# Optimization experiments

Measured on AMD Instinct MI355X. Metric: run time of the kernel, lower is better.

The kernel has to match this reference:

```python
import jax, jax.numpy as jnp
import numpy as np

RADIUS = 0.2
K = 32       # nsample
S = 1024     # npoint
BN_EPS = 1e-5


def fps(xyz, s):
    # xyz: [B, N, 3] -> indices [B, s] (farthest point sampling, start at index 0)
    B, N, _ = xyz.shape

    def step(carry, _):
        dist, last = carry                                  # [B,N], [B]
        lp = jnp.take_along_axis(xyz, last[:, None, None], axis=1)  # [B,1,3]
        d = jnp.sum((xyz - lp) ** 2, axis=-1)               # [B,N]
        dist = jnp.minimum(dist, d)
        nxt = jnp.argmax(dist, axis=-1).astype(jnp.int32)
        return (dist, nxt), last

    init = (jnp.full((B, N), jnp.inf, xyz.dtype), jnp.zeros((B,), jnp.int32))
    _, idxs = jax.lax.scan(step, init, None, length=s)      # [s, B]
    return idxs.T                                           # [B, s]


def query_ball(new_xyz, xyz, radius, k):
    # new_xyz: [B,S,3], xyz: [B,N,3] -> first k in-ball indices [B,S,k]
    B, N, _ = xyz.shape
    d2 = jnp.sum((new_xyz[:, :, None, :] - xyz[:, None, :, :]) ** 2, axis=-1)  # [B,S,N]
    cand = jnp.where(d2 <= radius * radius, jnp.arange(N, dtype=jnp.int32)[None, None, :], N)
    idx = jnp.sort(cand, axis=-1)[..., :k]                  # first-k by index, pytorch3d order
    first = idx[..., :1]
    idx = jnp.where(idx == N, first, idx)                   # replicate first valid index
    return jnp.minimum(idx, N - 1)


def gather_pts(pts, idx):
    # pts: [B,N,C], idx: [B,S,K] -> [B,S,K,C]
    B, N, C = pts.shape
    _, s, k = idx.shape
    g = jnp.take_along_axis(pts, idx.reshape(B, s * k, 1), axis=1)
    return g.reshape(B, s, k, C)


def conv_bn_relu(x, W, b, g, be):
    # x: [B,S,K,Cin], W: [Cout,Cin] (1x1 conv), training-mode BatchNorm over (B,S,K)
    y = jnp.einsum('bskc,oc->bsko', x, W) + b
    mu = jnp.mean(y, axis=(0, 1, 2))
    var = jnp.var(y, axis=(0, 1, 2))
    y = (y - mu) * jax.lax.rsqrt(var + BN_EPS) * g + be
    return jax.nn.relu(y)


def setup_inputs() -> dict:
    key = jax.random.key(0)
    ks = jax.random.split(key, 8)
    B, N, D = 8, 8192, 64
    inp = {
        'xyz': jax.random.uniform(ks[0], (B, 3, N), dtype=jnp.float32),
        'points': jax.random.normal(ks[1], (B, D, N), dtype=jnp.float32),
    }
    dims = [(64, 67), (64, 64), (128, 64)]
    for i, (o, c) in enumerate(dims):
        inp[f'W{i}'] = jax.random.normal(ks[2 + i], (o, c), dtype=jnp.float32) * 0.05
        inp[f'b{i}'] = jnp.zeros((o,), jnp.float32)
        inp[f'g{i}'] = jnp.ones((o,), jnp.float32)
        inp[f'be{i}'] = jnp.zeros((o,), jnp.float32)
    return inp


def reference(xyz, points, W0, b0, g0, be0, W1, b1, g1, be1, W2, b2, g2, be2):
    # xyz: [B,3,N], points: [B,D,N]
    xyz_n = jnp.transpose(xyz, (0, 2, 1))                   # [B,N,3]
    pts_n = jnp.transpose(points, (0, 2, 1))                # [B,N,D]
    idx = fps(xyz_n, S)                                     # [B,S]
    new_xyz = jnp.take_along_axis(xyz_n, idx[..., None], axis=1)  # [B,S,3]
    gidx = query_ball(new_xyz, xyz_n, RADIUS, K)            # [B,S,K]
    gxyz = (gather_pts(xyz_n, gidx) - new_xyz[:, :, None, :]) / RADIUS  # [B,S,K,3]
    gpts = gather_pts(pts_n, gidx)                          # [B,S,K,D]
    feat = jnp.concatenate([gpts, gxyz], axis=-1)           # [B,S,K,D+3]
    feat = conv_bn_relu(feat, W0, b0, g0, be0)
    feat = conv_bn_relu(feat, W1, b1, g1, be1)
    feat = conv_bn_relu(feat, W2, b2, g2, be2)
    new_points = jnp.max(feat, axis=2)                      # [B,S,Cout]
    return (jnp.transpose(new_xyz, (0, 2, 1)), jnp.transpose(new_points, (0, 2, 1)))
```

## Files before the change

kernel.cpp:

```cpp
#include <hip/hip_runtime.h>

#define BB 8
#define NN 8192
#define SS 1024
#define KK 32
#define NPIX (BB*SS*KK)
#define R2C 0.04f
#define EPS 1e-5f

#define FT 1024
#define FW (FT/64)
#define PPT (NN/FT)
#define NCELL 4096
#define TBLK 64

typedef float v2f __attribute__((ext_vector_type(2)));

#define OFF_IDX      0u
#define OFF_NEWXYZ   (OFF_IDX + BB*SS*4)
#define OFF_GIDX     (OFF_NEWXYZ + BB*SS*3*4)
#define OFF_XYZN     (OFF_GIDX + BB*SS*KK*4)
#define OFF_PTSN     (OFF_XYZN + BB*NN*3*4)
#define OFF_Y0       (OFF_PTSN + BB*NN*64*4)
#define OFF_Y1       (OFF_Y0 + NPIX*64*2)
#define OFF_MAXMIN   (OFF_Y1 + NPIX*64*2)
#define OFF_P0       (OFF_MAXMIN + BB*SS*128*2*4)
#define OFF_P1       (OFF_P0 + 1024*128*4)
#define OFF_P2       (OFF_P1 + 1024*128*4)
#define OFF_SC       (OFF_P2 + 1024*256*4)

__device__ __forceinline__ unsigned short f2bf(float x){
    unsigned u = __float_as_uint(x);
    unsigned r = (u + 0x7FFFu + ((u >> 16) & 1u)) >> 16;
    return (unsigned short)r;
}
__device__ __forceinline__ float bf2f(unsigned h){
    return __uint_as_float(h << 16);
}
__device__ __forceinline__ float sqdist3(float dx, float dy, float dz){
    return __fadd_rn(__fadd_rn(__fmul_rn(dx,dx), __fmul_rn(dy,dy)), __fmul_rn(dz,dz));
}
__device__ __forceinline__ int spread4(int v){
    return (v&1) | ((v&2)<<2) | ((v&4)<<4) | ((v&8)<<6);
}

template<int CTRL>
__device__ __forceinline__ unsigned long long dpp_max_u64(unsigned long long k){
    int lo = (int)(unsigned)k;
    int hi = (int)(unsigned)(k >> 32);
    int olo = __builtin_amdgcn_update_dpp(0, lo, CTRL, 0xf, 0xf, true);
    int ohi = __builtin_amdgcn_update_dpp(0, hi, CTRL, 0xf, 0xf, true);
    unsigned long long o = ((unsigned long long)(unsigned)ohi << 32) | (unsigned)olo;
    return (o > k) ? o : k;
}
template<int CTRL>
__device__ __forceinline__ float dppf_max(float v){
    int o = __builtin_amdgcn_update_dpp(__float_as_int(v), __float_as_int(v), CTRL, 0xf, 0xf, false);
    return fmaxf(v, __int_as_float(o));
}
template<int CTRL>
__device__ __forceinline__ float dppf_min(float v){
    int o = __builtin_amdgcn_update_dpp(__float_as_int(v), __float_as_int(v), CTRL, 0xf, 0xf, false);
    return fminf(v, __int_as_float(o));
}
template<int CTRL>
__device__ __forceinline__ unsigned dppu_min(unsigned v){
    unsigned o = (unsigned)__builtin_amdgcn_update_dpp((int)v, (int)v, CTRL, 0xf, 0xf, false);
    return min(v, o);
}
template<int CTRL>
__device__ __forceinline__ float dpp_sum_step(float v){
    int o = __builtin_amdgcn_update_dpp(0, __float_as_int(v), CTRL, 0xf, 0xf, true);
    return v + __int_as_float(o);
}
__device__ __forceinline__ float wave_sum_f32(float v){
    v = dpp_sum_step<0x111>(v); v = dpp_sum_step<0x112>(v);
    v = dpp_sum_step<0x114>(v); v = dpp_sum_step<0x118>(v);
    v = dpp_sum_step<0x142>(v); v = dpp_sum_step<0x143>(v);
    return v;
}
__device__ __forceinline__ float grp32_max(float v){
    v = dppf_max<0x111>(v); v = dppf_max<0x112>(v);
    v = dppf_max<0x114>(v); v = dppf_max<0x118>(v);
    v = dppf_max<0x142>(v);
    return v;
}
__device__ __forceinline__ float grp32_min(float v){
    v = dppf_min<0x111>(v); v = dppf_min<0x112>(v);
    v = dppf_min<0x114>(v); v = dppf_min<0x118>(v);
    v = dppf_min<0x142>(v);
    return v;
}
__device__ __forceinline__ float wave_max_f32(float v){
    v = dppf_max<0x111>(v); v = dppf_max<0x112>(v);
    v = dppf_max<0x114>(v); v = dppf_max<0x118>(v);
    v = dppf_max<0x142>(v); v = dppf_max<0x143>(v);
    return v;
}
__device__ __forceinline__ unsigned wave_min_u32(unsigned v){
    v = dppu_min<0x111>(v); v = dppu_min<0x112>(v);
    v = dppu_min<0x114>(v); v = dppu_min<0x118>(v);
    v = dppu_min<0x142>(v); v = dppu_min<0x143>(v);
    return v;
}

__global__ __launch_bounds__(FT) void fps_kernel(const float* __restrict__ xyz,
                                                 const float* __restrict__ pts,
                                                 float* __restrict__ newxyz,
                                                 float* __restrict__ out,
                                                 float* __restrict__ xyz_n,
                                                 float* __restrict__ pts_n){
    __shared__ float sxyz[NN * 3];
    __shared__ int   si[NN];
    __shared__ int   hist[NCELL];
    __shared__ int   waveTot[FW];
    __shared__ unsigned long long slots[2][FW];
    int tid = threadIdx.x;

    if (blockIdx.x >= 8){
        int gid = (blockIdx.x - 8) * FT + tid;
        int b = gid >> 13, i = gid & (NN - 1);
        const float* xb = xyz + (size_t)b * 3 * NN;
        float x = xb[i], y = xb[NN + i], z = xb[2 * NN + i];
        float* xd = xyz_n + ((size_t)b * NN + i) * 3;
        xd[0] = x; xd[1] = y; xd[2] = z;
        const float* pb = pts + (size_t)b * 64 * NN + i;
        float4* pd = (float4*)(pts_n + ((size_t)b * NN + i) * 64);
#pragma unroll
        for (int q = 0; q < 16; ++q){
            float4 v;
            v.x = pb[(q*4+0)*NN]; v.y = pb[(q*4+1)*NN];
            v.z = pb[(q*4+2)*NN]; v.w = pb[(q*4+3)*NN];
            pd[q] = v;
        }
        return;
    }

    int b = blockIdx.x;
    int wave = tid >> 6, lane = tid & 63;
    const float* xb = xyz + (size_t)b * 3 * NN;

    int cell[PPT];
#pragma unroll
    for (int j = 0; j < PPT; ++j){
        int i = tid + j * FT;
        float x = xb[i], y = xb[NN + i], z = xb[2*NN + i];
        sxyz[i*3]   = x; sxyz[i*3+1] = y; sxyz[i*3+2] = z;
        int cx = min(15, max(0, (int)(x * 16.f)));
        int cy = min(15, max(0, (int)(y * 16.f)));
        int cz = min(15, max(0, (int)(z * 16.f)));
        cell[j] = spread4(cx) | (spread4(cy) << 1) | (spread4(cz) << 2);
    }
#pragma unroll
    for (int k = 0; k < NCELL/FT; ++k) hist[tid * (NCELL/FT) + k] = 0;
    __syncthreads();
#pragma unroll
    for (int j = 0; j < PPT; ++j) atomicAdd(&hist[cell[j]], 1);
    __syncthreads();
    {
        int base0 = tid * (NCELL/FT);
        int sum4 = 0;
#pragma unroll
        for (int k = 0; k < NCELL/FT; ++k) sum4 += hist[base0 + k];
        int s = sum4;
#pragma unroll
        for (int m = 1; m < 64; m <<= 1){
            int v = __shfl_up(s, m);
            if (lane >= m) s += v;
        }
        if (lane == 63) waveTot[wave] = s;
        __syncthreads();
        int wbase = 0;
#pragma unroll
        for (int w2 = 0; w2 < FW; ++w2) if (w2 < wave) wbase += waveTot[w2];
        int run = wbase + s - sum4;
#pragma unroll
        for (int k = 0; k < NCELL/FT; ++k){
            int h = hist[base0 + k];
            hist[base0 + k] = run;
            run += h;
        }
    }
    __syncthreads();
#pragma unroll
    for (int j = 0; j < PPT; ++j){
        int pos = atomicAdd(&hist[cell[j]], 1);
        si[pos] = tid + j * FT;
    }
    __syncthreads();
    v2f px[PPT/2], py[PPT/2], pz[PPT/2];
    float dist[PPT];
    int oi[PPT];
    float bxmin =  1e30f, bxmax = -1e30f;
    float bymin =  1e30f, bymax = -1e30f;
    float bzmin =  1e30f, bzmax = -1e30f;
#pragma unroll
    for (int j = 0; j < PPT; ++j){
        int g = si[tid * PPT + j];
        oi[j] = g;
        float x = sxyz[g*3], y = sxyz[g*3+1], z = sxyz[g*3+2];
        px[j>>1][j&1] = x; py[j>>1][j&1] = y; pz[j>>1][j&1] = z;
        bxmin = fminf(bxmin, x); bxmax = fmaxf(bxmax, x);
        bymin = fminf(bymin, y); bymax = fmaxf(bymax, y);
        bzmin = fminf(bzmin, z); bzmax = fmaxf(bzmax, z);
        dist[j] = __int_as_float(0x7f800000);
    }
    __syncthreads();

    float tmax = __int_as_float(0x7f800000);
    int   bidx = 0;
    unsigned long long wkey = 0ull;
    int w = 0;
    for (int t = 0; t < SS; ++t){
        if (tid == 0) hist[t] = w;
        int w3 = w * 3;
        float lx = sxyz[w3], ly = sxyz[w3+1], lz = sxyz[w3+2];
        float cdx = __fsub_rn(lx, fminf(fmaxf(lx, bxmin), bxmax));
        float cdy = __fsub_rn(ly, fminf(fmaxf(ly, bymin), bymax));
        float cdz = __fsub_rn(lz, fminf(fmaxf(lz, bzmin), bzmax));
        float d_bb = sqdist3(cdx, cdy, cdz);
        bool active = d_bb < tmax;
        unsigned long long bal = __ballot(active);
        if (bal){
            if (active){
                {
#pragma clang fp contract(off)
                    v2f lx2 = {lx, lx}, ly2 = {ly, ly}, lz2 = {lz, lz};
#pragma unroll
                    for (int p = 0; p < PPT/2; ++p){
                        v2f dx = px[p] - lx2;
                        v2f dy = py[p] - ly2;
                        v2f dz = pz[p] - lz2;
                        v2f d  = ((dx*dx) + (dy*dy)) + (dz*dz);
                        dist[2*p]   = fminf(dist[2*p],   d[0]);
                        dist[2*p+1] = fminf(dist[2*p+1], d[1]);
                    }
                }
                float m0 = fmaxf(dist[0], dist[1]);
                float m1 = fmaxf(dist[2], dist[3]);
                float m2 = fmaxf(dist[4], dist[5]);
                float m3 = fmaxf(dist[6], dist[7]);
                m0 = fmaxf(m0, m1); m2 = fmaxf(m2, m3);
                float maxd = fmaxf(m0, m2);
                int bo = 0x7fffffff;
#pragma unroll
                for (int j = 0; j < PPT; ++j)
                    if (dist[j] == maxd) bo = min(bo, oi[j]);
                tmax = maxd; bidx = bo;
            }
            float m = wave_max_f32(tmax);
            float sm = __int_as_float(__builtin_amdgcn_readlane(__float_as_int(m), 63));
            unsigned cand = (tmax == sm) ? (unsigned)bidx : 0xFFFFFFFFu;
            cand = wave_min_u32(cand);
            unsigned sidx = (unsigned)__builtin_amdgcn_readlane((int)cand, 63);
            wkey = ((unsigned long long)__float_as_uint(sm) << 32) | (unsigned)(~sidx);
        }
        int cur = t & 1;
        if (lane == 63) slots[cur][wave] = wkey;
        __syncthreads();
        unsigned long long v = (lane < FW) ? slots[cur][lane] : 0ull;
        v = dpp_max_u64<0x111>(v);
        v = dpp_max_u64<0x112>(v);
        v = dpp_max_u64<0x114>(v);
        v = dpp_max_u64<0x118>(v);
        unsigned lo = (unsigned)__builtin_amdgcn_readlane((int)(unsigned)v, 15);
        w = (int)(~lo);
    }
    __syncthreads();
    for (int t2 = tid; t2 < SS; t2 += FT){
        int hw = hist[t2] * 3;
        float x = sxyz[hw], y = sxyz[hw+1], z = sxyz[hw+2];
        out[(size_t)b * 3 * SS + t2]          = x;
        out[(size_t)b * 3 * SS + SS + t2]     = y;
        out[(size_t)b * 3 * SS + 2*SS + t2]   = z;
        float* nw = newxyz + ((size_t)b * SS + t2) * 3;
        nw[0] = x; nw[1] = y; nw[2] = z;
    }
}

__global__ __launch_bounds__(256) void qb_kernel(const float* __restrict__ xyz,
                                                 const float* __restrict__ newxyz,
                                                 int* __restrict__ gidx){
    int wid = (blockIdx.x * 256 + threadIdx.x) >> 6;
    int lane = threadIdx.x & 63;
    int b = wid >> 10;
    const float* nw = newxyz + (size_t)wid * 3;
    float cx = nw[0], cy = nw[1], cz = nw[2];
    const float* xb = xyz + (size_t)b * 3 * NN;
    int total = 0, firstIdx = -1;
    int* gout = gidx + (size_t)wid * KK;
    for (int base = 0; base < NN; base += 64){
        int i = base + lane;
        float dx = __fsub_rn(cx, xb[i]);
        float dy = __fsub_rn(cy, xb[NN + i]);
        float dz = __fsub_rn(cz, xb[2*NN + i]);
        float d2 = sqdist3(dx, dy, dz);
        bool in = (d2 <= R2C);
        unsigned long long m = __ballot(in);
        int pos = total + __popcll(m & ((1ull << lane) - 1ull));
        if (in && pos < KK) gout[pos] = i;
        if (firstIdx < 0 && m) firstIdx = base + (__ffsll((unsigned long long)m) - 1);
        total += __popcll(m);
        if (total >= KK) break;
    }
    if (total < KK){
        int f = (total > 0) ? firstIdx : (NN - 1);
        for (int p = total + lane; p < KK; p += 64) gout[p] = f;
    }
}

__global__ __launch_bounds__(256) void l0_kernel(const float* __restrict__ pts_n,
                                                 const float* __restrict__ xyz_n,
                                                 const float* __restrict__ newxyz,
                                                 const int* __restrict__ gidx,
                                                 const float* __restrict__ W0,
                                                 const float* __restrict__ b0,
                                                 uint4* __restrict__ y0,
                                                 float* __restrict__ part0){
    __shared__ float lsum[4][64][2];
    int tid = threadIdx.x;
    int pixel = blockIdx.x * 256 + tid;
    int sample = pixel >> 5;
    int b = sample >> 10;
    int gi = gidx[pixel];
    int wave = tid >> 6, lane = tid & 63;

    float ff[67];
    const float4* prow = (const float4*)(pts_n + ((size_t)b * NN + gi) * 64);
#pragma unroll
    for (int q = 0; q < 16; ++q){
        float4 v = prow[q];
        ff[q*4] = v.x; ff[q*4+1] = v.y; ff[q*4+2] = v.z; ff[q*4+3] = v.w;
    }
    const float* pr = xyz_n + ((size_t)b * NN + gi) * 3;
    const float* nw = newxyz + (size_t)sample * 3;
    ff[64] = __fsub_rn(pr[0], nw[0]) / 0.2f;
    ff[65] = __fsub_rn(pr[1], nw[1]) / 0.2f;
    ff[66] = __fsub_rn(pr[2], nw[2]) / 0.2f;

    for (int oc = 0; oc < 8; ++oc){
        float acc[8];
#pragma unroll
        for (int j = 0; j < 8; ++j) acc[j] = b0[oc*8+j];
#pragma unroll
        for (int c = 0; c < 67; ++c){
            float fe = ff[c];
#pragma unroll
            for (int j = 0; j < 8; ++j) acc[j] += fe * W0[(oc*8+j)*67 + c];
        }
        uint4 pk;
        unsigned us[8];
#pragma unroll
        for (int j = 0; j < 8; ++j){
            float v = acc[j];
            float s1 = wave_sum_f32(v);
            float s2 = wave_sum_f32(v * v);
            if (lane == 63){ lsum[wave][oc*8+j][0] = s1; lsum[wave][oc*8+j][1] = s2; }
            us[j] = f2bf(v);
        }
        pk.x = us[0] | (us[1] << 16);
        pk.y = us[2] | (us[3] << 16);
        pk.z = us[4] | (us[5] << 16);
        pk.w = us[6] | (us[7] << 16);
        y0[(size_t)pixel * 8 + oc] = pk;
    }
    __syncthreads();
    if (tid < 128){
        float s = lsum[0][tid>>1][tid&1] + lsum[1][tid>>1][tid&1]
                + lsum[2][tid>>1][tid&1] + lsum[3][tid>>1][tid&1];
        part0[(size_t)blockIdx.x * 128 + tid] = s;
    }
}

__global__ __launch_bounds__(256) void l1_kernel(const uint4* __restrict__ y0,
                                                 const float* __restrict__ scale0,
                                                 const float* __restrict__ shift0,
                                                 const float* __restrict__ W1,
                                                 const float* __restrict__ b1,
                                                 uint4* __restrict__ y1,
                                                 float* __restrict__ part1){
    __shared__ float lsum[4][64][2];
    int tid = threadIdx.x;
    int pixel = blockIdx.x * 256 + tid;
    int wave = tid >> 6, lane = tid & 63;

    float x[64];
#pragma unroll
    for (int q = 0; q < 8; ++q){
        uint4 v = y0[(size_t)pixel * 8 + q];
        unsigned w[4] = {v.x, v.y, v.z, v.w};
#pragma unroll
        for (int r = 0; r < 4; ++r){
            int c = q*8 + r*2;
            x[c]   = fmaxf(bf2f(w[r] & 0xFFFFu) * scale0[c]   + shift0[c],   0.f);
            x[c+1] = fmaxf(bf2f(w[r] >> 16)     * scale0[c+1] + shift0[c+1], 0.f);
        }
    }
    for (int oc = 0; oc < 8; ++oc){
        float acc[8];
#pragma unroll
        for (int j = 0; j < 8; ++j) acc[j] = b1[oc*8+j];
#pragma unroll
        for (int c = 0; c < 64; ++c){
            float fe = x[c];
#pragma unroll
            for (int j = 0; j < 8; ++j) acc[j] += fe * W1[(oc*8+j)*64 + c];
        }
        uint4 pk;
        unsigned us[8];
#pragma unroll
        for (int j = 0; j < 8; ++j){
            float v = acc[j];
            float s1 = wave_sum_f32(v);
            float s2 = wave_sum_f32(v * v);
            if (lane == 63){ lsum[wave][oc*8+j][0] = s1; lsum[wave][oc*8+j][1] = s2; }
            us[j] = f2bf(v);
        }
        pk.x = us[0] | (us[1] << 16);
        pk.y = us[2] | (us[3] << 16);
        pk.z = us[4] | (us[5] << 16);
        pk.w = us[6] | (us[7] << 16);
        y1[(size_t)pixel * 8 + oc] = pk;
    }
    __syncthreads();
    if (tid < 128){
        float s = lsum[0][tid>>1][tid&1] + lsum[1][tid>>1][tid&1]
                + lsum[2][tid>>1][tid&1] + lsum[3][tid>>1][tid&1];
        part1[(size_t)blockIdx.x * 128 + tid] = s;
    }
}

__global__ __launch_bounds__(256) void l2_kernel(const uint4* __restrict__ y1,
                                                 const float* __restrict__ scale1,
                                                 const float* __restrict__ shift1,
                                                 const float* __restrict__ W2,
                                                 const float* __restrict__ b2,
                                                 float* __restrict__ maxmin,
                                                 float* __restrict__ part2){
    __shared__ float lsum[4][128][2];
    int tid = threadIdx.x;
    int pixel = blockIdx.x * 256 + tid;
    int sample = pixel >> 5;
    int wave = tid >> 6, lane = tid & 63;

    float x[64];
#pragma unroll
    for (int q = 0; q < 8; ++q){
        uint4 v = y1[(size_t)pixel * 8 + q];
        unsigned w[4] = {v.x, v.y, v.z, v.w};
#pragma unroll
        for (int r = 0; r < 4; ++r){
            int c = q*8 + r*2;
            x[c]   = fmaxf(bf2f(w[r] & 0xFFFFu) * scale1[c]   + shift1[c],   0.f);
            x[c+1] = fmaxf(bf2f(w[r] >> 16)     * scale1[c+1] + shift1[c+1], 0.f);
        }
    }
    for (int oc = 0; oc < 16; ++oc){
        float acc[8];
#pragma unroll
        for (int j = 0; j < 8; ++j) acc[j] = b2[oc*8+j];
#pragma unroll
        for (int c = 0; c < 64; ++c){
            float fe = x[c];
#pragma unroll
            for (int j = 0; j < 8; ++j) acc[j] += fe * W2[(oc*8+j)*64 + c];
        }
#pragma unroll
        for (int j = 0; j < 8; ++j){
            float v = acc[j];
            int ch = oc*8 + j;
            float mx = grp32_max(v);
            float mn = grp32_min(v);
            float s1 = wave_sum_f32(v);
            float s2 = wave_sum_f32(v * v);
            if (lane == 63){ lsum[wave][ch][0] = s1; lsum[wave][ch][1] = s2; }
            if ((tid & 31) == 31){
                float* mm = maxmin + ((size_t)sample * 128 + ch) * 2;
                mm[0] = mx; mm[1] = mn;
            }
        }
    }
    __syncthreads();
    {
        float s = lsum[0][tid>>1][tid&1] + lsum[1][tid>>1][tid&1]
                + lsum[2][tid>>1][tid&1] + lsum[3][tid>>1][tid&1];
        part2[(size_t)blockIdx.x * 256 + tid] = s;
    }
}

__global__ __launch_bounds__(1024) void fin_kernel(const float* __restrict__ part, int O,
                           const float* __restrict__ g, const float* __restrict__ be,
                           float* __restrict__ scale, float* __restrict__ shift){
    __shared__ float4 ls[1024];
    int tid = threadIdx.x;
    int M = 2 * O;
    int V = M >> 2;
    int NC = 1024 / V;
    int q = tid & (V - 1);
    int c = tid / V;
    int per = 1024 / NC;
    const float4* p4 = (const float4*)part;
    float4 s = {0.f, 0.f, 0.f, 0.f};
    for (int r = 0; r < per; ++r){
        int blk = c * per + r;
        float4 v = p4[(size_t)blk * V + q];
        s.x += v.x; s.y += v.y; s.z += v.z; s.w += v.w;
    }
    ls[c * V + q] = s;
    __syncthreads();
    if (tid < V){
        float4 t4 = ls[tid];
        for (int c2 = 1; c2 < NC; ++c2){
            float4 v = ls[c2 * V + tid];
            t4.x += v.x; t4.y += v.y; t4.z += v.z; t4.w += v.w;
        }
        float inv = 1.0f / (float)NPIX;
        int ch0 = 2 * tid, ch1 = 2 * tid + 1;
        float mu0 = t4.x * inv;
        float var0 = t4.y * inv - mu0 * mu0;
        float sc0 = (1.0f / sqrtf(var0 + EPS)) * g[ch0];
        scale[ch0] = sc0; shift[ch0] = be[ch0] - mu0 * sc0;
        float mu1 = t4.z * inv;
        float var1 = t4.w * inv - mu1 * mu1;
        float sc1 = (1.0f / sqrtf(var1 + EPS)) * g[ch1];
        scale[ch1] = sc1; shift[ch1] = be[ch1] - mu1 * sc1;
    }
}

__global__ __launch_bounds__(256) void out_kernel(const float* __restrict__ maxmin,
                                                  const float* __restrict__ scale2,
                                                  const float* __restrict__ shift2,
                                                  float* __restrict__ out){
    int gid = blockIdx.x * 256 + threadIdx.x;
    int s = gid & 1023;
    int o = (gid >> 10) & 127;
    int b = gid >> 17;
    int sample = b * 1024 + s;
    float2 mm = ((const float2*)maxmin)[(size_t)sample * 128 + o];
    float sc = scale2[o], sh = shift2[o];
    float v = (sc >= 0.f) ? mm.x : mm.y;
    out[gid] = fmaxf(v * sc + sh, 0.f);
}

extern "C" void kernel_launch(void* const* d_in, const int* in_sizes, int n_in,
                              void* d_out, int out_size, void* d_ws, size_t ws_size,
                              hipStream_t stream) {
    const float* xyz = (const float*)d_in[0];
    const float* pts = (const float*)d_in[1];
    const float* W0 = (const float*)d_in[2];
    const float* b0 = (const float*)d_in[3];
    const float* g0 = (const float*)d_in[4];
    const float* be0 = (const float*)d_in[5];
    const float* W1 = (const float*)d_in[6];
    const float* b1 = (const float*)d_in[7];
    const float* g1 = (const float*)d_in[8];
    const float* be1 = (const float*)d_in[9];
    const float* W2 = (const float*)d_in[10];
    const float* b2 = (const float*)d_in[11];
    const float* g2 = (const float*)d_in[12];
    const float* be2 = (const float*)d_in[13];

    char* ws = (char*)d_ws;
    float* newxyz = (float*)(ws + OFF_NEWXYZ);
    int*   gidx   = (int*)(ws + OFF_GIDX);
    float* xyz_n  = (float*)(ws + OFF_XYZN);
    float* pts_n  = (float*)(ws + OFF_PTSN);
    uint4* y0     = (uint4*)(ws + OFF_Y0);
    uint4* y1     = (uint4*)(ws + OFF_Y1);
    float* maxmin = (float*)(ws + OFF_MAXMIN);
    float* part0  = (float*)(ws + OFF_P0);
    float* part1  = (float*)(ws + OFF_P1);
    float* part2  = (float*)(ws + OFF_P2);
    float* sc     = (float*)(ws + OFF_SC);
    float* scale0 = sc,        *shift0 = sc + 64;
    float* scale1 = sc + 128,  *shift1 = sc + 192;
    float* scale2 = sc + 256,  *shift2 = sc + 384;

    float* out = (float*)d_out;
    float* out_np = out + BB * 3 * SS;

    hipLaunchKernelGGL(fps_kernel, dim3(8 + TBLK), dim3(FT), 0, stream,
                       xyz, pts, newxyz, out, xyz_n, pts_n);
    hipLaunchKernelGGL(qb_kernel, dim3(2048), dim3(256), 0, stream, xyz, newxyz, gidx);
    hipLaunchKernelGGL(l0_kernel, dim3(1024), dim3(256), 0, stream,
                       pts_n, xyz_n, newxyz, gidx, W0, b0, y0, part0);
    hipLaunchKernelGGL(fin_kernel, dim3(1), dim3(1024), 0, stream, part0, 64, g0, be0, scale0, shift0);
    hipLaunchKernelGGL(l1_kernel, dim3(1024), dim3(256), 0, stream,
                       y0, scale0, shift0, W1, b1, y1, part1);
    hipLaunchKernelGGL(fin_kernel, dim3(1), dim3(1024), 0, stream, part1, 64, g1, be1, scale1, shift1);
    hipLaunchKernelGGL(l2_kernel, dim3(1024), dim3(256), 0, stream,
                       y1, scale1, shift1, W2, b2, maxmin, part2);
    hipLaunchKernelGGL(fin_kernel, dim3(1), dim3(1024), 0, stream, part2, 128, g2, be2, scale2, shift2);
    hipLaunchKernelGGL(out_kernel, dim3(4096), dim3(256), 0, stream, maxmin, scale2, shift2, out_np);
}
```

Before: 1.329 ms.

## Fuse ball query into layer 0, fold BN finalize into last blocks, atomicMax FPS reduce

Moves the ball-query search into the layer-0 conv kernel, so the gathered indices stay in shared memory and no longer round-trip through global memory. The three single-block BN finalize kernels are replaced by a last-block-done pattern: an atomic counter picks the final block, which reduces the partial sums. The FPS per-step cross-wave reduction now uses a shared-memory 64-bit atomicMax per step instead of slot writes plus a DPP reduction. This removes four kernel launches but adds threadfence and atomic overhead, and the tail reduction now runs in a 256-thread block instead of 1024.

New measurement: 1.502 ms. +13.1%, slower.

```diff
diff --git a/kernel.cpp b/kernel.cpp
--- a/kernel.cpp
+++ b/kernel.cpp
@@ -28,6 +28,7 @@
 #define OFF_P1       (OFF_P0 + 1024*128*4)
 #define OFF_P2       (OFF_P1 + 1024*128*4)
 #define OFF_SC       (OFF_P2 + 1024*256*4)
+#define OFF_CNT      (OFF_SC + 512*4)
 
 __device__ __forceinline__ unsigned short f2bf(float x){
     unsigned u = __float_as_uint(x);
@@ -44,15 +45,6 @@
     return (v&1) | ((v&2)<<2) | ((v&4)<<4) | ((v&8)<<6);
 }
 
-template<int CTRL>
-__device__ __forceinline__ unsigned long long dpp_max_u64(unsigned long long k){
-    int lo = (int)(unsigned)k;
-    int hi = (int)(unsigned)(k >> 32);
-    int olo = __builtin_amdgcn_update_dpp(0, lo, CTRL, 0xf, 0xf, true);
-    int ohi = __builtin_amdgcn_update_dpp(0, hi, CTRL, 0xf, 0xf, true);
-    unsigned long long o = ((unsigned long long)(unsigned)ohi << 32) | (unsigned)olo;
-    return (o > k) ? o : k;
-}
 template<int CTRL>
 __device__ __forceinline__ float dppf_max(float v){
     int o = __builtin_amdgcn_update_dpp(__float_as_int(v), __float_as_int(v), CTRL, 0xf, 0xf, false);
@@ -109,15 +101,17 @@
                                                  float* __restrict__ newxyz,
                                                  float* __restrict__ out,
                                                  float* __restrict__ xyz_n,
-                                                 float* __restrict__ pts_n){
+                                                 float* __restrict__ pts_n,
+                                                 int* __restrict__ cnt){
     __shared__ float sxyz[NN * 3];
     __shared__ int   si[NN];
     __shared__ int   hist[NCELL];
     __shared__ int   waveTot[FW];
-    __shared__ unsigned long long slots[2][FW];
+    __shared__ unsigned long long cells[SS];
     int tid = threadIdx.x;
 
     if (blockIdx.x >= 8){
+        if (blockIdx.x == 8 && tid < 4) cnt[tid] = 0;
         int gid = (blockIdx.x - 8) * FT + tid;
         int b = gid >> 13, i = gid & (NN - 1);
         const float* xb = xyz + (size_t)b * 3 * NN;
@@ -153,6 +147,7 @@
     }
 #pragma unroll
     for (int k = 0; k < NCELL/FT; ++k) hist[tid * (NCELL/FT) + k] = 0;
+    cells[tid] = 0ull;
     __syncthreads();
 #pragma unroll
     for (int j = 0; j < PPT; ++j) atomicAdd(&hist[cell[j]], 1);
@@ -255,16 +250,9 @@
             unsigned sidx = (unsigned)__builtin_amdgcn_readlane((int)cand, 63);
             wkey = ((unsigned long long)__float_as_uint(sm) << 32) | (unsigned)(~sidx);
         }
-        int cur = t & 1;
-        if (lane == 63) slots[cur][wave] = wkey;
+        if (lane == 63) atomicMax(&cells[t], wkey);
         __syncthreads();
-        unsigned long long v = (lane < FW) ? slots[cur][lane] : 0ull;
-        v = dpp_max_u64<0x111>(v);
-        v = dpp_max_u64<0x112>(v);
-        v = dpp_max_u64<0x114>(v);
-        v = dpp_max_u64<0x118>(v);
-        unsigned lo = (unsigned)__builtin_amdgcn_readlane((int)(unsigned)v, 15);
-        w = (int)(~lo);
+        w = (int)(~(unsigned)cells[t]);
     }
     __syncthreads();
     for (int t2 = tid; t2 < SS; t2 += FT){
@@ -278,52 +266,90 @@
     }
 }
 
-__global__ __launch_bounds__(256) void qb_kernel(const float* __restrict__ xyz,
-                                                 const float* __restrict__ newxyz,
-                                                 int* __restrict__ gidx){
-    int wid = (blockIdx.x * 256 + threadIdx.x) >> 6;
-    int lane = threadIdx.x & 63;
-    int b = wid >> 10;
-    const float* nw = newxyz + (size_t)wid * 3;
-    float cx = nw[0], cy = nw[1], cz = nw[2];
-    const float* xb = xyz + (size_t)b * 3 * NN;
-    int total = 0, firstIdx = -1;
-    int* gout = gidx + (size_t)wid * KK;
-    for (int base = 0; base < NN; base += 64){
-        int i = base + lane;
-        float dx = __fsub_rn(cx, xb[i]);
-        float dy = __fsub_rn(cy, xb[NN + i]);
-        float dz = __fsub_rn(cz, xb[2*NN + i]);
-        float d2 = sqdist3(dx, dy, dz);
-        bool in = (d2 <= R2C);
-        unsigned long long m = __ballot(in);
-        int pos = total + __popcll(m & ((1ull << lane) - 1ull));
-        if (in && pos < KK) gout[pos] = i;
-        if (firstIdx < 0 && m) firstIdx = base + (__ffsll((unsigned long long)m) - 1);
-        total += __popcll(m);
-        if (total >= KK) break;
-    }
-    if (total < KK){
-        int f = (total > 0) ? firstIdx : (NN - 1);
-        for (int p = total + lane; p < KK; p += 64) gout[p] = f;
-    }
-}
-
-__global__ __launch_bounds__(256) void l0_kernel(const float* __restrict__ pts_n,
+__device__ void fin_tail(const float* __restrict__ part, int O,
+                         const float* __restrict__ g, const float* __restrict__ be,
+                         float* __restrict__ scale, float* __restrict__ shift,
+                         float* fs){
+    int tid = threadIdx.x;
+    int M = 2 * O;
+    int nch = 256 / M;
+    int m = tid & (M - 1);
+    int chunk = tid / M;
+    int per = 1024 / nch;
+    float s = 0.f;
+    for (int r = 0; r < per; ++r)
+        s += part[(size_t)(chunk * per + r) * M + m];
+    fs[tid] = s;
+    __syncthreads();
+    if (tid < M){
+        float t = fs[tid];
+        for (int c = 1; c < nch; ++c) t += fs[c * M + tid];
+        fs[tid] = t;
+    }
+    __syncthreads();
+    if (tid < O){
+        float s1 = fs[2*tid], s2 = fs[2*tid+1];
+        float inv = 1.0f / (float)NPIX;
+        float mu = s1 * inv;
+        float var = s2 * inv - mu * mu;
+        float sc = (1.0f / sqrtf(var + EPS)) * g[tid];
+        scale[tid] = sc;
+        shift[tid] = be[tid] - mu * sc;
+    }
+}
+
+__global__ __launch_bounds__(256) void l0_kernel(const float* __restrict__ xyz,
+                                                 const float* __restrict__ pts_n,
                                                  const float* __restrict__ xyz_n,
                                                  const float* __restrict__ newxyz,
-                                                 const int* __restrict__ gidx,
                                                  const float* __restrict__ W0,
                                                  const float* __restrict__ b0,
+                                                 const float* __restrict__ g0,
+                                                 const float* __restrict__ be0,
                                                  uint4* __restrict__ y0,
-                                                 float* __restrict__ part0){
+                                                 float* __restrict__ part0,
+                                                 float* __restrict__ scale0,
+                                                 float* __restrict__ shift0,
+                                                 int* __restrict__ cnt0){
     __shared__ float lsum[4][64][2];
+    __shared__ int   gq[8][KK];
+    __shared__ int   lastFlag;
     int tid = threadIdx.x;
+    int wave = tid >> 6, lane = tid & 63;
+    int b = blockIdx.x >> 7;
+
+    const float* xb = xyz + (size_t)b * 3 * NN;
+#pragma unroll
+    for (int s2 = 0; s2 < 2; ++s2){
+        int ls = wave * 2 + s2;
+        int sample = blockIdx.x * 8 + ls;
+        const float* nw = newxyz + (size_t)sample * 3;
+        float cx = nw[0], cy = nw[1], cz = nw[2];
+        int total = 0, firstIdx = -1;
+        for (int base = 0; base < NN; base += 64){
+            int i = base + lane;
+            float dx = __fsub_rn(cx, xb[i]);
+            float dy = __fsub_rn(cy, xb[NN + i]);
+            float dz = __fsub_rn(cz, xb[2*NN + i]);
+            float d2 = sqdist3(dx, dy, dz);
+            bool in = (d2 <= R2C);
+            unsigned long long m = __ballot(in);
+            int pos = total + __popcll(m & ((1ull << lane) - 1ull));
+            if (in && pos < KK) gq[ls][pos] = i;
+            if (firstIdx < 0 && m) firstIdx = base + (__ffsll((unsigned long long)m) - 1);
+            total += __popcll(m);
+            if (total >= KK) break;
+        }
+        if (total < KK){
+            int f = (total > 0) ? firstIdx : (NN - 1);
+            for (int p = total + lane; p < KK; p += 64) gq[ls][p] = f;
+        }
+    }
+    __syncthreads();
+
     int pixel = blockIdx.x * 256 + tid;
     int sample = pixel >> 5;
-    int b = sample >> 10;
-    int gi = gidx[pixel];
-    int wave = tid >> 6, lane = tid & 63;
+    int gi = gq[tid >> 5][tid & 31];
 
     float ff[67];
     const float4* prow = (const float4*)(pts_n + ((size_t)b * NN + gi) * 64);
@@ -370,6 +396,17 @@
                 + lsum[2][tid>>1][tid&1] + lsum[3][tid>>1][tid&1];
         part0[(size_t)blockIdx.x * 128 + tid] = s;
     }
+    __threadfence();
+    __syncthreads();
+    if (tid == 0){
+        int c = atomicAdd(cnt0, 1);
+        lastFlag = (c == (int)gridDim.x - 1);
+    }
+    __syncthreads();
+    if (lastFlag){
+        __threadfence();
+        fin_tail(part0, 64, g0, be0, scale0, shift0, (float*)lsum);
+    }
 }
 
 __global__ __launch_bounds__(256) void l1_kernel(const uint4* __restrict__ y0,
@@ -377,9 +414,15 @@
                                                  const float* __restrict__ shift0,
                                                  const float* __restrict__ W1,
                                                  const float* __restrict__ b1,
+                                                 const float* __restrict__ g1,
+                                                 const float* __restrict__ be1,
                                                  uint4* __restrict__ y1,
-                                                 float* __restrict__ part1){
+                                                 float* __restrict__ part1,
+                                                 float* __restrict__ scale1,
+                                                 float* __restrict__ shift1,
+                                                 int* __restrict__ cnt1){
     __shared__ float lsum[4][64][2];
+    __shared__ int lastFlag;
     int tid = threadIdx.x;
     int pixel = blockIdx.x * 256 + tid;
     int wave = tid >> 6, lane = tid & 63;
@@ -428,6 +471,17 @@
                 + lsum[2][tid>>1][tid&1] + lsum[3][tid>>1][tid&1];
         part1[(size_t)blockIdx.x * 128 + tid] = s;
     }
+    __threadfence();
+    __syncthreads();
+    if (tid == 0){
+        int c = atomicAdd(cnt1, 1);
+        lastFlag = (c == (int)gridDim.x - 1);
+    }
+    __syncthreads();
+    if (lastFlag){
+        __threadfence();
+        fin_tail(part1, 64, g1, be1, scale1, shift1, (float*)lsum);
+    }
 }
 
 __global__ __launch_bounds__(256) void l2_kernel(const uint4* __restrict__ y1,
@@ -435,9 +489,15 @@
                                                  const float* __restrict__ shift1,
                                                  const float* __restrict__ W2,
                                                  const float* __restrict__ b2,
+                                                 const float* __restrict__ g2,
+                                                 const float* __restrict__ be2,
                                                  float* __restrict__ maxmin,
-                                                 float* __restrict__ part2){
+                                                 float* __restrict__ part2,
+                                                 float* __restrict__ scale2,
+                                                 float* __restrict__ shift2,
+                                                 int* __restrict__ cnt2){
     __shared__ float lsum[4][128][2];
+    __shared__ int lastFlag;
     int tid = threadIdx.x;
     int pixel = blockIdx.x * 256 + tid;
     int sample = pixel >> 5;
@@ -486,44 +546,16 @@
                 + lsum[2][tid>>1][tid&1] + lsum[3][tid>>1][tid&1];
         part2[(size_t)blockIdx.x * 256 + tid] = s;
     }
-}
-
-__global__ __launch_bounds__(1024) void fin_kernel(const float* __restrict__ part, int O,
-                           const float* __restrict__ g, const float* __restrict__ be,
-                           float* __restrict__ scale, float* __restrict__ shift){
-    __shared__ float4 ls[1024];
-    int tid = threadIdx.x;
-    int M = 2 * O;
-    int V = M >> 2;
-    int NC = 1024 / V;
-    int q = tid & (V - 1);
-    int c = tid / V;
-    int per = 1024 / NC;
-    const float4* p4 = (const float4*)part;
-    float4 s = {0.f, 0.f, 0.f, 0.f};
-    for (int r = 0; r < per; ++r){
-        int blk = c * per + r;
-        float4 v = p4[(size_t)blk * V + q];
-        s.x += v.x; s.y += v.y; s.z += v.z; s.w += v.w;
-    }
-    ls[c * V + q] = s;
-    __syncthreads();
-    if (tid < V){
-        float4 t4 = ls[tid];
-        for (int c2 = 1; c2 < NC; ++c2){
-            float4 v = ls[c2 * V + tid];
-            t4.x += v.x; t4.y += v.y; t4.z += v.z; t4.w += v.w;
-        }
-        float inv = 1.0f / (float)NPIX;
-        int ch0 = 2 * tid, ch1 = 2 * tid + 1;
-        float mu0 = t4.x * inv;
-        float var0 = t4.y * inv - mu0 * mu0;
-        float sc0 = (1.0f / sqrtf(var0 + EPS)) * g[ch0];
-        scale[ch0] = sc0; shift[ch0] = be[ch0] - mu0 * sc0;
-        float mu1 = t4.z * inv;
-        float var1 = t4.w * inv - mu1 * mu1;
-        float sc1 = (1.0f / sqrtf(var1 + EPS)) * g[ch1];
-        scale[ch1] = sc1; shift[ch1] = be[ch1] - mu1 * sc1;
+    __threadfence();
+    __syncthreads();
+    if (tid == 0){
+        int c = atomicAdd(cnt2, 1);
+        lastFlag = (c == (int)gridDim.x - 1);
+    }
+    __syncthreads();
+    if (lastFlag){
+        __threadfence();
+        fin_tail(part2, 128, g2, be2, scale2, shift2, (float*)lsum);
     }
 }
 
@@ -562,7 +594,6 @@
 
     char* ws = (char*)d_ws;
     float* newxyz = (float*)(ws + OFF_NEWXYZ);
-    int*   gidx   = (int*)(ws + OFF_GIDX);
     float* xyz_n  = (float*)(ws + OFF_XYZN);
     float* pts_n  = (float*)(ws + OFF_PTSN);
     uint4* y0     = (uint4*)(ws + OFF_Y0);
@@ -575,21 +606,22 @@
     float* scale0 = sc,        *shift0 = sc + 64;
     float* scale1 = sc + 128,  *shift1 = sc + 192;
     float* scale2 = sc + 256,  *shift2 = sc + 384;
+    int*   cnt    = (int*)(ws + OFF_CNT);
 
     float* out = (float*)d_out;
     float* out_np = out + BB * 3 * SS;
 
     hipLaunchKernelGGL(fps_kernel, dim3(8 + TBLK), dim3(FT), 0, stream,
-                       xyz, pts, newxyz, out, xyz_n, pts_n);
-    hipLaunchKernelGGL(qb_kernel, dim3(2048), dim3(256), 0, stream, xyz, newxyz, gidx);
+                       xyz, pts, newxyz, out, xyz_n, pts_n, cnt);
     hipLaunchKernelGGL(l0_kernel, dim3(1024), dim3(256), 0, stream,
-                       pts_n, xyz_n, newxyz, gidx, W0, b0, y0, part0);
-    hipLaunchKernelGGL(fin_kernel, dim3(1), dim3(1024), 0, stream, part0, 64, g0, be0, scale0, shift0);
+                       xyz, pts_n, xyz_n, newxyz, W0, b0, g0, be0,
+                       y0, part0, scale0, shift0, cnt + 0);
     hipLaunchKernelGGL(l1_kernel, dim3(1024), dim3(256), 0, stream,
-                       y0, scale0, shift0, W1, b1, y1, part1);
-    hipLaunchKernelGGL(fin_kernel, dim3(1), dim3(1024), 0, stream, part1, 64, g1, be1, scale1, shift1);
+                       y0, scale0, shift0, W1, b1, g1, be1,
+                       y1, part1, scale1, shift1, cnt + 1);
     hipLaunchKernelGGL(l2_kernel, dim3(1024), dim3(256), 0, stream,
-                       y1, scale1, shift1, W2, b2, maxmin, part2);
-    hipLaunchKernelGGL(fin_kernel, dim3(1), dim3(1024), 0, stream, part2, 128, g2, be2, scale2, shift2);
-    hipLaunchKernelGGL(out_kernel, dim3(4096), dim3(256), 0, stream, maxmin, scale2, shift2, out_np);
-}
+                       y1, scale1, shift1, W2, b2, g2, be2,
+                       maxmin, part2, scale2, shift2, cnt + 2);
+    hipLaunchKernelGGL(out_kernel, dim3(4096), dim3(256), 0, stream,
+                       maxmin, scale2, shift2, out_np);
+}
```
